# Performance work log

Hardware: AMD Instinct MI355X
Metric: run time of the kernel (lower is better)

## Reference

```python
import jax, jax.numpy as jnp
import numpy as np

N_NODES = 50000
N_EDGES = 800000
N_GRAPHS = 256
F_IN = 75  # num_features_xd


def _lin_params(key, fan_in, fan_out):
    kw, kb = jax.random.split(key)
    s = 1.0 / np.sqrt(fan_in)
    W = jax.random.uniform(kw, (fan_in, fan_out), jnp.float32, -s, s)
    b = jax.random.uniform(kb, (fan_out,), jnp.float32, -s, s)
    return W, b


def setup_inputs() -> dict:
    key = jax.random.key(0)
    ks = jax.random.split(key, 8)
    x = jax.random.normal(ks[0], (N_NODES, F_IN), jnp.float32)
    edge_index = jax.random.randint(ks[1], (2, N_EDGES), 0, N_NODES, jnp.int32)
    batch = jnp.sort(jax.random.randint(ks[2], (N_NODES,), 0, N_GRAPHS, jnp.int32))
    W1, b1 = _lin_params(ks[3], F_IN, F_IN)            # conv1: 75 -> 75
    W2, b2 = _lin_params(ks[4], F_IN, 2 * F_IN)        # conv2: 75 -> 150
    W3, b3 = _lin_params(ks[5], 2 * F_IN, 4 * F_IN)    # conv3: 150 -> 300
    Wg1, bg1 = _lin_params(ks[6], 4 * F_IN, 1024)      # fc_g1: 300 -> 1024
    Wg2, bg2 = _lin_params(ks[7], 1024, 128)           # fc_g2: 1024 -> 128
    return dict(x=x, edge_index=edge_index, batch=batch,
                W1=W1, b1=b1, W2=W2, b2=b2, W3=W3, b3=b3,
                Wg1=Wg1, bg1=bg1, Wg2=Wg2, bg2=bg2)


def gcn_conv(x, W, b, src, dst, n):
    """PyG GCNConv: out = D^{-1/2}(A+I)D^{-1/2} X W + b (symmetric norm, self loops)."""
    h = x @ W                                   # [n, out]
    loop = jnp.arange(n, dtype=src.dtype)
    s = jnp.concatenate([src, loop])            # [E+n]
    d = jnp.concatenate([dst, loop])
    deg = jax.ops.segment_sum(jnp.ones(s.shape[0], x.dtype), d, num_segments=n)
    dinv = jnp.where(deg > 0, jax.lax.rsqrt(jnp.maximum(deg, 1e-12)), 0.0)
    norm = dinv[s] * dinv[d]                    # [E+n]
    out = jax.ops.segment_sum(norm[:, None] * h[s], d, num_segments=n)
    return out + b


def reference(x, edge_index, batch, W1, b1, W2, b2, W3, b3, Wg1, bg1, Wg2, bg2):
    src, dst = edge_index[0], edge_index[1]
    n = x.shape[0]
    h = jax.nn.relu(gcn_conv(x, W1, b1, src, dst, n))
    h = jax.nn.relu(gcn_conv(h, W2, b2, src, dst, n))
    h = jax.nn.relu(gcn_conv(h, W3, b3, src, dst, n))
    g = jax.ops.segment_max(h, batch, num_segments=N_GRAPHS)  # global max pool
    g = jax.nn.relu(g @ Wg1 + bg1)
    # dropout is identity in eval mode
    return g @ Wg2 + bg2
```

## Files before the change

kernel.cpp:

```cpp
#include <hip/hip_runtime.h>
#include <math.h>

#define SCAN_B 1024
#define LDST 40

typedef __attribute__((ext_vector_type(8))) short short8v;
typedef __attribute__((ext_vector_type(8))) unsigned short ushort8v;
typedef __attribute__((ext_vector_type(4))) float f32x4;

static inline int ceil_div_i(long long a, int b) { return (int)((a + b - 1) / b); }

__device__ __forceinline__ unsigned short f2bf(float x) {
    unsigned int u = __float_as_uint(x);
    u += 0x7fffu + ((u >> 16) & 1u);
    return (unsigned short)(u >> 16);
}
__device__ __forceinline__ float bf2f(unsigned short h) {
    return __uint_as_float(((unsigned int)h) << 16);
}


__global__ __launch_bounds__(256) void k_count(const int* __restrict__ dst, int E,
                                               int* __restrict__ cnt) {
    int i = blockIdx.x * blockDim.x + threadIdx.x;
    if (i < E) atomicAdd(&cnt[dst[i]], 1);
}

__global__ __launch_bounds__(256) void k_dinv(const int* __restrict__ cnt,
                                              float* __restrict__ dinv, int N) {
    int i = blockIdx.x * blockDim.x + threadIdx.x;
    if (i < N) dinv[i] = (float)(1.0 / sqrt((double)(cnt[i] + 1)));
}

__global__ __launch_bounds__(256) void k_scan1(const int* __restrict__ cnt,
                                               int* __restrict__ rowptr,
                                               int* __restrict__ bsum, int N) {
    __shared__ int s[256];
    int tid = threadIdx.x;
    int base = blockIdx.x * SCAN_B + tid * 4;
    int a0 = (base + 0 < N) ? cnt[base + 0] : 0;
    int a1 = (base + 1 < N) ? cnt[base + 1] : 0;
    int a2 = (base + 2 < N) ? cnt[base + 2] : 0;
    int a3 = (base + 3 < N) ? cnt[base + 3] : 0;
    int tsum = a0 + a1 + a2 + a3;
    s[tid] = tsum;
    __syncthreads();
    for (int off = 1; off < 256; off <<= 1) {
        int val = 0;
        if (tid >= off) val = s[tid - off];
        __syncthreads();
        if (tid >= off) s[tid] += val;
        __syncthreads();
    }
    int texcl = s[tid] - tsum;
    if (tid == 255) bsum[blockIdx.x] = s[255];
    if (base + 0 < N) rowptr[base + 0] = texcl;
    if (base + 1 < N) rowptr[base + 1] = texcl + a0;
    if (base + 2 < N) rowptr[base + 2] = texcl + a0 + a1;
    if (base + 3 < N) rowptr[base + 3] = texcl + a0 + a1 + a2;
}

__global__ __launch_bounds__(256) void k_scan2(int* __restrict__ bsum, int NB) {
    __shared__ int s[256];
    int tid = threadIdx.x;
    int v = (tid < NB) ? bsum[tid] : 0;
    s[tid] = v;
    __syncthreads();
    for (int off = 1; off < 256; off <<= 1) {
        int val = 0;
        if (tid >= off) val = s[tid - off];
        __syncthreads();
        if (tid >= off) s[tid] += val;
        __syncthreads();
    }
    if (tid < NB) bsum[tid] = s[tid] - v;
}

__global__ __launch_bounds__(256) void k_scan3(int* __restrict__ rowptr,
                                               const int* __restrict__ bsum, int N, int E) {
    int i = blockIdx.x * blockDim.x + threadIdx.x;
    if (i < N) rowptr[i] += bsum[i >> 10];
    if (i == 0) rowptr[N] = E;
}

__global__ __launch_bounds__(256) void k_fill(const int* __restrict__ src,
                                              const int* __restrict__ dst, int E,
                                              const int* __restrict__ rowptr,
                                              int* __restrict__ fill,
                                              int* __restrict__ col) {
    int e = blockIdx.x * blockDim.x + threadIdx.x;
    if (e >= E) return;
    int s = src[e], d = dst[e];
    int pos = atomicAdd(&fill[d], 1);
    col[rowptr[d] + pos] = s;
}


__global__ __launch_bounds__(256) void k_xscale(const float* __restrict__ x,
                                                const float* __restrict__ dinv,
                                                unsigned short* __restrict__ xb,
                                                int N, int F, int XS) {
    int i = blockIdx.x * blockDim.x + threadIdx.x;
    int v = i / XS, c = i - v * XS;
    if (v >= N) return;
    float val = (c < F) ? dinv[v] * x[(size_t)v * F + c] : 0.f;
    xb[i] = f2bf(val);
}


template <int CHUNKS, int SLOTS, int UNR>
__global__ __launch_bounds__(256) void k_gather_s(const unsigned short* __restrict__ Xb,
                                                  const int* __restrict__ rowptr,
                                                  const int* __restrict__ col,
                                                  float* __restrict__ T, int N,
                                                  int XS, int KPf) {
    const int v = blockIdx.x * 4 + (threadIdx.x >> 6);
    const int lane = threadIdx.x & 63;
    if (v >= N) return;
    constexpr int VW = 8;
    const int slot = lane / CHUNKS;
    const int chunk = lane - slot * CHUNKS;
    const bool act = lane < CHUNKS * SLOTS;
    const int f0 = chunk * VW;

    float acc[VW];
#pragma unroll
    for (int u = 0; u < VW; u++) acc[u] = 0.f;
    if (slot == 0) {
        ushort8v h = *(const ushort8v*)(Xb + (size_t)v * XS + f0);
#pragma unroll
        for (int u = 0; u < VW; u++) acc[u] = bf2f(h[u]);
    }

    const int beg = rowptr[v], end = rowptr[v + 1];
    for (int jb = beg; jb < end; jb += 64) {
        const int nj = min(64, end - jb);
        int ec = 0;
        if (lane < nj) ec = col[jb + lane];
        for (int e = 0; e < nj; e += SLOTS * UNR) {
            int cs[UNR];
            bool vs[UNR];
#pragma unroll
            for (int u = 0; u < UNR; u++) {
                int srcl = e + u * SLOTS + slot;
                vs[u] = act && (srcl < nj);
                cs[u] = __shfl(ec, srcl & 63);
            }
            ushort8v xv[UNR];
#pragma unroll
            for (int u = 0; u < UNR; u++) {
#pragma unroll
                for (int k2 = 0; k2 < 8; k2++) xv[u][k2] = 0;
                if (vs[u]) xv[u] = *(const ushort8v*)(Xb + (size_t)cs[u] * XS + f0);
            }
#pragma unroll
            for (int u = 0; u < UNR; u++)
#pragma unroll
                for (int k2 = 0; k2 < VW; k2++)
                    acc[k2] += bf2f(xv[u][k2]);
        }
    }

#pragma unroll
    for (int k2 = 0; k2 < VW; k2++) {
        float t2 = acc[k2];
#pragma unroll
        for (int s2 = 1; s2 < SLOTS; s2++) t2 += __shfl(acc[k2], chunk + s2 * CHUNKS);
        acc[k2] = t2;
    }

    if (slot == 0 && f0 < KPf) {
        float* tv = T + (size_t)v * KPf + f0;
        f32x4 o0 = {acc[0], acc[1], acc[2], acc[3]};
        f32x4 o1 = {acc[4], acc[5], acc[6], acc[7]};
        *(f32x4*)tv = o0;
        *(f32x4*)(tv + 4) = o1;
    }
}


__global__ __launch_bounds__(256) void k_wsplit(const float* __restrict__ W,
                                                unsigned short* __restrict__ Wth,
                                                unsigned short* __restrict__ Wtl,
                                                int K, int Fout, int KP) {
    int i = blockIdx.x * blockDim.x + threadIdx.x;
    if (i >= Fout * KP) return;
    int c = i / KP, k = i - c * KP;
    float w = (k < K) ? W[(size_t)k * Fout + c] : 0.f;
    unsigned short h = f2bf(w);
    Wth[i] = h;
    Wtl[i] = f2bf(w - bf2f(h));
}


template <int MODE>
__global__ __launch_bounds__(256) void k_gemm_mfma(
    const float* __restrict__ A, int KPf,
    const unsigned short* __restrict__ Bth, const unsigned short* __restrict__ Btl,
    const float* __restrict__ bias, const float* __restrict__ dinvp,
    unsigned short* __restrict__ Cb, int CSbf,
    const int* __restrict__ batch, float* __restrict__ G,
    int N, int KP, int Fout) {
    __shared__ unsigned short sAh[128 * LDST];
    __shared__ unsigned short sAl[128 * LDST];
    __shared__ unsigned short sBh[128 * LDST];
    __shared__ unsigned short sBl[128 * LDST];
    __shared__ int sBatch[128];

    const int t = threadIdx.x;
    const int r0 = blockIdx.x * 128;
    const int c0 = blockIdx.y * 128;
    const int lane = t & 63;
    const int wv = t >> 6;
    const int wrow = (wv >> 1) * 64;
    const int wcol = (wv & 1) * 64;
    const int l15 = lane & 15;
    const int lk = (lane >> 4) * 8;
    const int nt = KP >> 5;

    const int srow = t >> 1;
    const int sseg = (t & 1) << 4;

    if (MODE == 1 && t < 128) sBatch[t] = (r0 + t < N) ? batch[r0 + t] : -1;

    const bool arow_ok = (r0 + srow) < N;
    const bool bcol_ok = (c0 + srow) < Fout;
    const float* aRow = A + (size_t)(r0 + srow) * KPf;
    const unsigned short* bhRow = Bth + (size_t)(c0 + srow) * KP;
    const unsigned short* blRow = Btl + (size_t)(c0 + srow) * KP;

    float av[16];
    ushort8v rbh0, rbh1, rbl0, rbl1;

    auto gload = [&](int kk) {
#pragma unroll
        for (int u = 0; u < 4; u++) {
            int gk = kk + sseg + u * 4;
            f32x4 f = {0.f, 0.f, 0.f, 0.f};
            if (arow_ok && gk < KPf) f = *(const f32x4*)&aRow[gk];
#pragma unroll
            for (int e = 0; e < 4; e++) av[u * 4 + e] = f[e];
        }
        if (bcol_ok) {
            const ushort8v* p = (const ushort8v*)&bhRow[kk + sseg];
            rbh0 = p[0];
            rbh1 = p[1];
            p = (const ushort8v*)&blRow[kk + sseg];
            rbl0 = p[0];
            rbl1 = p[1];
        } else {
#pragma unroll
            for (int e = 0; e < 8; e++) { rbh0[e] = 0; rbh1[e] = 0; rbl0[e] = 0; rbl1[e] = 0; }
        }
    };

    auto wlds = [&]() {
        int off = srow * LDST + sseg;
        ushort8v h0, h1, l0, l1;
#pragma unroll
        for (int e = 0; e < 8; e++) {
            unsigned short hh = f2bf(av[e]);
            h0[e] = hh;
            l0[e] = f2bf(av[e] - bf2f(hh));
        }
#pragma unroll
        for (int e = 0; e < 8; e++) {
            unsigned short hh = f2bf(av[8 + e]);
            h1[e] = hh;
            l1[e] = f2bf(av[8 + e] - bf2f(hh));
        }
        *(ushort8v*)&sAh[off] = h0;
        *(ushort8v*)&sAh[off + 8] = h1;
        *(ushort8v*)&sAl[off] = l0;
        *(ushort8v*)&sAl[off + 8] = l1;
        *(ushort8v*)&sBh[off] = rbh0;
        *(ushort8v*)&sBh[off + 8] = rbh1;
        *(ushort8v*)&sBl[off] = rbl0;
        *(ushort8v*)&sBl[off + 8] = rbl1;
    };

    f32x4 acc[4][4];
#pragma unroll
    for (int i = 0; i < 4; i++)
#pragma unroll
        for (int j = 0; j < 4; j++) acc[i][j] = (f32x4){0.f, 0.f, 0.f, 0.f};

    gload(0);
    for (int tc = 0; tc < nt; ++tc) {
        wlds();
        __syncthreads();
        if (tc + 1 < nt) gload((tc + 1) * 32);
        short8v ah[4], al[4];
#pragma unroll
        for (int i = 0; i < 4; i++) {
            int ro = (wrow + i * 16 + l15) * LDST + lk;
            ah[i] = *(const short8v*)&sAh[ro];
            al[i] = *(const short8v*)&sAl[ro];
        }
#pragma unroll
        for (int j = 0; j < 4; j++) {
            int co = (wcol + j * 16 + l15) * LDST + lk;
            short8v bh = *(const short8v*)&sBh[co];
            short8v bl = *(const short8v*)&sBl[co];
#pragma unroll
            for (int i = 0; i < 4; i++) {
                acc[i][j] = __builtin_amdgcn_mfma_f32_16x16x32_bf16(al[i], bh, acc[i][j], 0, 0, 0);
                acc[i][j] = __builtin_amdgcn_mfma_f32_16x16x32_bf16(ah[i], bl, acc[i][j], 0, 0, 0);
                acc[i][j] = __builtin_amdgcn_mfma_f32_16x16x32_bf16(ah[i], bh, acc[i][j], 0, 0, 0);
            }
        }
        __syncthreads();
    }

    float drw[16];
#pragma unroll
    for (int i = 0; i < 4; i++)
#pragma unroll
        for (int q = 0; q < 4; q++) {
            int gr = r0 + wrow + i * 16 + (lane >> 4) * 4 + q;
            drw[i * 4 + q] = (gr < N) ? dinvp[gr] : 0.f;
        }

    if (MODE == 0) {
#pragma unroll
        for (int j = 0; j < 4; j++) {
            int gc = c0 + wcol + j * 16 + l15;
            if (gc >= CSbf) continue;
            float bv = (gc < Fout) ? bias[gc] : 0.f;
#pragma unroll
            for (int i = 0; i < 4; i++) {
                int rb = r0 + wrow + i * 16 + (lane >> 4) * 4;
#pragma unroll
                for (int q = 0; q < 4; q++) {
                    int gr = rb + q;
                    if (gr >= N) continue;
                    float dr = drw[i * 4 + q];
                    float vv = (gc < Fout) ? fmaxf(fmaf(acc[i][j][q], dr, bv), 0.f) * dr : 0.f;
                    Cb[(size_t)gr * CSbf + gc] = f2bf(vv);
                }
            }
        }
    } else {
#pragma unroll
        for (int j = 0; j < 4; j++) {
            int gc = c0 + wcol + j * 16 + l15;
            if (gc >= Fout) continue;
            float bv = bias[gc];
            int gcur = -1;
            float vmax = 0.f;
#pragma unroll
            for (int i = 0; i < 4; i++) {
                int lr = wrow + i * 16 + (lane >> 4) * 4;
#pragma unroll
                for (int q = 0; q < 4; q++) {
                    int g = sBatch[lr + q];
                    float vv = fmaxf(fmaf(acc[i][j][q], drw[i * 4 + q], bv), 0.f);
                    if (g < 0) continue;
                    if (g != gcur) {
                        if (gcur >= 0)
                            atomicMax((int*)&G[(size_t)gcur * Fout + gc], __float_as_int(vmax));
                        gcur = g;
                        vmax = vv;
                    } else {
                        vmax = fmaxf(vmax, vv);
                    }
                }
            }
            if (gcur >= 0) atomicMax((int*)&G[(size_t)gcur * Fout + gc], __float_as_int(vmax));
        }
    }
}


__global__ __launch_bounds__(256) void k_fc1(const float* __restrict__ A,
                                             const float* __restrict__ W,
                                             const float* __restrict__ bias,
                                             float* __restrict__ C,
                                             int M, int K, int Nout) {
    __shared__ float sA[2 * 304];
    const int t = threadIdx.x;
    const int m0 = blockIdx.x * 2;
    const int oc = blockIdx.y * 256 + t;

    for (int i = t; i < 2 * K; i += 256) {
        int r = i / K, k = i - r * K;
        sA[r * 304 + k] = (m0 + r < M) ? A[(size_t)(m0 + r) * K + k] : 0.f;
    }
    __syncthreads();

    float acc0 = 0.f, acc1 = 0.f;
    int k = 0;
    for (; k + 8 <= K; k += 8) {
        float w[8];
#pragma unroll
        for (int u = 0; u < 8; u++) w[u] = W[(size_t)(k + u) * Nout + oc];
#pragma unroll
        for (int u = 0; u < 8; u++) {
            acc0 = fmaf(sA[k + u], w[u], acc0);
            acc1 = fmaf(sA[304 + k + u], w[u], acc1);
        }
    }
    for (; k < K; k++) {
        float w = W[(size_t)k * Nout + oc];
        acc0 = fmaf(sA[k], w, acc0);
        acc1 = fmaf(sA[304 + k], w, acc1);
    }
    float bv = bias[oc];
    if (m0 < M) C[(size_t)m0 * Nout + oc] = fmaxf(acc0 + bv, 0.f);
    if (m0 + 1 < M) C[(size_t)(m0 + 1) * Nout + oc] = fmaxf(acc1 + bv, 0.f);
}


__global__ __launch_bounds__(256) void k_fc2p(const float* __restrict__ A,
                                              const float* __restrict__ W,
                                              float* __restrict__ P,
                                              int M, int K, int Nout) {
    __shared__ float sA[2 * 256];
    const int t = threadIdx.x;
    const int m0 = blockIdx.x * 2;
    const int sk = blockIdx.y;
    const int k0 = sk * 256;
    const int row = t >> 7;
    const int oc = t & 127;

    for (int i = t; i < 2 * 256; i += 256) {
        int r = i >> 8, k = i & 255;
        sA[i] = (m0 + r < M) ? A[(size_t)(m0 + r) * K + k0 + k] : 0.f;
    }
    __syncthreads();

    const float* a = sA + row * 256;
    float acc = 0.f;
    for (int k = 0; k < 256; k += 8) {
        float w[8];
#pragma unroll
        for (int u = 0; u < 8; u++) w[u] = W[(size_t)(k0 + k + u) * Nout + oc];
#pragma unroll
        for (int u = 0; u < 8; u++) acc = fmaf(a[k + u], w[u], acc);
    }
    int m = m0 + row;
    if (m < M) P[((size_t)sk * M + m) * Nout + oc] = acc;
}

__global__ __launch_bounds__(256) void k_fc2r(const float* __restrict__ P,
                                              const float* __restrict__ bias,
                                              float* __restrict__ C,
                                              int M, int Nout, int SK) {
    int i = blockIdx.x * blockDim.x + threadIdx.x;
    if (i >= M * Nout) return;
    int oc = i % Nout;
    float acc = bias[oc];
    for (int s2 = 0; s2 < SK; s2++) acc += P[(size_t)s2 * M * Nout + i];
    C[i] = acc;
}


extern "C" void kernel_launch(void* const* d_in, const int* in_sizes, int n_in,
                              void* d_out, int out_size, void* d_ws, size_t ws_size,
                              hipStream_t stream) {
    const float* x     = (const float*)d_in[0];
    const int*   ei    = (const int*)d_in[1];
    const int*   batch = (const int*)d_in[2];
    const float* W1 = (const float*)d_in[3];
    const float* b1 = (const float*)d_in[4];
    const float* W2 = (const float*)d_in[5];
    const float* b2 = (const float*)d_in[6];
    const float* W3 = (const float*)d_in[7];
    const float* b3 = (const float*)d_in[8];
    const float* Wg1 = (const float*)d_in[9];
    const float* bg1 = (const float*)d_in[10];
    const float* Wg2 = (const float*)d_in[11];
    const float* bg2 = (const float*)d_in[12];

    const int N  = in_sizes[2];
    const int E  = in_sizes[1] / 2;
    const int F1 = in_sizes[4];
    const int F2 = in_sizes[6];
    const int F3 = in_sizes[8];
    const int H1 = in_sizes[10];
    const int OC = in_sizes[12];
    const int NG = out_size / OC;
    const int FIN = in_sizes[3] / F1;

    const int KP1 = 96,  KPf1 = 80;
    const int KP3 = 160, KPf3 = 152;
    const int XS0 = 80;
    const int HS1 = 80;
    const int HS2 = 152;

    const int* src = ei;
    const int* dst = ei + E;

    char* base = (char*)d_ws;
    size_t off = 0;
    auto alloc = [&](size_t bytes) -> void* {
        void* p = base + off;
        off = (off + bytes + 255) & ~(size_t)255;
        return p;
    };
    int*   cnt    = (int*)alloc((size_t)N * 4);
    int*   fill   = (int*)alloc((size_t)N * 4);
    int*   rowptr = (int*)alloc((size_t)(N + 1) * 4);
    float* dinv   = (float*)alloc((size_t)N * 4);
    int*   bsum   = (int*)alloc(256 * 4);
    int*   col    = (int*)alloc((size_t)E * 4);
    unsigned short* W1th = (unsigned short*)alloc((size_t)F1 * KP1 * 2);
    unsigned short* W1tl = (unsigned short*)alloc((size_t)F1 * KP1 * 2);
    unsigned short* W2th = (unsigned short*)alloc((size_t)F2 * KP1 * 2);
    unsigned short* W2tl = (unsigned short*)alloc((size_t)F2 * KP1 * 2);
    unsigned short* W3th = (unsigned short*)alloc((size_t)F3 * KP3 * 2);
    unsigned short* W3tl = (unsigned short*)alloc((size_t)F3 * KP3 * 2);
    float* Gb  = (float*)alloc((size_t)NG * F3 * 4);
    float* g1  = (float*)alloc((size_t)NG * H1 * 4);
    float* P2  = (float*)alloc((size_t)4 * NG * OC * 4);
    float* Tg  = (float*)alloc((size_t)N * KPf3 * 4);
    unsigned short* Xb  = (unsigned short*)alloc((size_t)N * XS0 * 2);
    unsigned short* H1b = (unsigned short*)alloc((size_t)N * HS1 * 2);
    unsigned short* H2b = (unsigned short*)alloc((size_t)N * HS2 * 2);

    hipMemsetAsync(cnt, 0, (size_t)N * 4, stream);
    hipMemsetAsync(fill, 0, (size_t)N * 4, stream);
    hipMemsetAsync(Gb, 0, (size_t)NG * F3 * 4, stream);

    k_count<<<ceil_div_i(E, 256), 256, 0, stream>>>(dst, E, cnt);
    k_dinv<<<ceil_div_i(N, 256), 256, 0, stream>>>(cnt, dinv, N);
    int NB = ceil_div_i(N, SCAN_B);
    k_scan1<<<NB, 256, 0, stream>>>(cnt, rowptr, bsum, N);
    k_scan2<<<1, 256, 0, stream>>>(bsum, NB);
    k_scan3<<<ceil_div_i(N, 256), 256, 0, stream>>>(rowptr, bsum, N, E);
    k_fill<<<ceil_div_i(E, 256), 256, 0, stream>>>(src, dst, E, rowptr, fill, col);

    k_wsplit<<<ceil_div_i((long long)F1 * KP1, 256), 256, 0, stream>>>(W1, W1th, W1tl, FIN, F1, KP1);
    k_wsplit<<<ceil_div_i((long long)F2 * KP1, 256), 256, 0, stream>>>(W2, W2th, W2tl, F1, F2, KP1);
    k_wsplit<<<ceil_div_i((long long)F3 * KP3, 256), 256, 0, stream>>>(W3, W3th, W3tl, F2, F3, KP3);
    k_xscale<<<ceil_div_i((long long)N * XS0, 256), 256, 0, stream>>>(x, dinv, Xb, N, FIN, XS0);

    dim3 blk(256);
    int gw = ceil_div_i(N, 4);
    int gx = ceil_div_i(N, 128);

    k_gather_s<10, 6, 2><<<gw, blk, 0, stream>>>(Xb, rowptr, col, Tg, N, XS0, KPf1);
    {
        dim3 g(gx, ceil_div_i(F1, 128));
        k_gemm_mfma<0><<<g, blk, 0, stream>>>(Tg, KPf1, W1th, W1tl, b1, dinv, H1b, HS1,
                                              nullptr, nullptr, N, KP1, F1);
    }
    k_gather_s<10, 6, 2><<<gw, blk, 0, stream>>>(H1b, rowptr, col, Tg, N, HS1, KPf1);
    {
        dim3 g(gx, ceil_div_i(F2, 128));
        k_gemm_mfma<0><<<g, blk, 0, stream>>>(Tg, KPf1, W2th, W2tl, b2, dinv, H2b, HS2,
                                              nullptr, nullptr, N, KP1, F2);
    }
    k_gather_s<19, 3, 4><<<gw, blk, 0, stream>>>(H2b, rowptr, col, Tg, N, HS2, KPf3);
    {
        dim3 g(gx, ceil_div_i(F3, 128));
        k_gemm_mfma<1><<<g, blk, 0, stream>>>(Tg, KPf3, W3th, W3tl, b3, dinv, nullptr, 0,
                                              batch, Gb, N, KP3, F3);
    }

    {
        dim3 g(ceil_div_i(NG, 2), H1 / 256);
        k_fc1<<<g, 256, 0, stream>>>(Gb, Wg1, bg1, g1, NG, F3, H1);
    }
    {
        dim3 g(ceil_div_i(NG, 2), 4);
        k_fc2p<<<g, 256, 0, stream>>>(g1, Wg2, P2, NG, H1, OC);
        k_fc2r<<<ceil_div_i((long long)NG * OC, 256), 256, 0, stream>>>(
            P2, bg2, (float*)d_out, NG, OC, 4);
    }
}
```

Baseline: 336.3 us.

## Emit bf16 hi/lo split from gather and use MFMA-fragment LDS layout in GEMM

```diff
diff --git a/kernel.cpp b/kernel.cpp
--- a/kernel.cpp
+++ b/kernel.cpp
@@ -2,7 +2,6 @@
 #include <math.h>
 
 #define SCAN_B 1024
-#define LDST 40
 
 typedef __attribute__((ext_vector_type(8))) short short8v;
 typedef __attribute__((ext_vector_type(8))) unsigned short ushort8v;
@@ -17,6 +16,12 @@
 }
 __device__ __forceinline__ float bf2f(unsigned short h) {
     return __uint_as_float(((unsigned int)h) << 16);
+}
+__device__ __forceinline__ ushort8v zero8() {
+    ushort8v z;
+#pragma unroll
+    for (int e = 0; e < 8; e++) z[e] = 0;
+    return z;
 }
 
 
@@ -112,8 +117,9 @@
 __global__ __launch_bounds__(256) void k_gather_s(const unsigned short* __restrict__ Xb,
                                                   const int* __restrict__ rowptr,
                                                   const int* __restrict__ col,
-                                                  float* __restrict__ T, int N,
-                                                  int XS, int KPf) {
+                                                  unsigned short* __restrict__ Th,
+                                                  unsigned short* __restrict__ Tl,
+                                                  int N, int XS, int KPf) {
     const int v = blockIdx.x * 4 + (threadIdx.x >> 6);
     const int lane = threadIdx.x & 63;
     if (v >= N) return;
@@ -149,8 +155,7 @@
             ushort8v xv[UNR];
 #pragma unroll
             for (int u = 0; u < UNR; u++) {
-#pragma unroll
-                for (int k2 = 0; k2 < 8; k2++) xv[u][k2] = 0;
+                xv[u] = zero8();
                 if (vs[u]) xv[u] = *(const ushort8v*)(Xb + (size_t)cs[u] * XS + f0);
             }
 #pragma unroll
@@ -170,11 +175,15 @@
     }
 
     if (slot == 0 && f0 < KPf) {
-        float* tv = T + (size_t)v * KPf + f0;
-        f32x4 o0 = {acc[0], acc[1], acc[2], acc[3]};
-        f32x4 o1 = {acc[4], acc[5], acc[6], acc[7]};
-        *(f32x4*)tv = o0;
-        *(f32x4*)(tv + 4) = o1;
+        ushort8v h8, l8;
+#pragma unroll
+        for (int u = 0; u < VW; u++) {
+            unsigned short hh = f2bf(acc[u]);
+            h8[u] = hh;
+            l8[u] = f2bf(acc[u] - bf2f(hh));
+        }
+        *(ushort8v*)(Th + (size_t)v * KPf + f0) = h8;
+        *(ushort8v*)(Tl + (size_t)v * KPf + f0) = l8;
     }
 }
 
@@ -195,16 +204,16 @@
 
 template <int MODE>
 __global__ __launch_bounds__(256) void k_gemm_mfma(
-    const float* __restrict__ A, int KPf,
+    const unsigned short* __restrict__ Ah, const unsigned short* __restrict__ Al, int KPf,
     const unsigned short* __restrict__ Bth, const unsigned short* __restrict__ Btl,
     const float* __restrict__ bias, const float* __restrict__ dinvp,
     unsigned short* __restrict__ Cb, int CSbf,
     const int* __restrict__ batch, float* __restrict__ G,
     int N, int KP, int Fout) {
-    __shared__ unsigned short sAh[128 * LDST];
-    __shared__ unsigned short sAl[128 * LDST];
-    __shared__ unsigned short sBh[128 * LDST];
-    __shared__ unsigned short sBl[128 * LDST];
+    __shared__ unsigned short sAh[128 * 32];
+    __shared__ unsigned short sAl[128 * 32];
+    __shared__ unsigned short sBh[128 * 32];
+    __shared__ unsigned short sBl[128 * 32];
     __shared__ int sBatch[128];
 
     const int t = threadIdx.x;
@@ -215,68 +224,53 @@
     const int wrow = (wv >> 1) * 64;
     const int wcol = (wv & 1) * 64;
     const int l15 = lane & 15;
-    const int lk = (lane >> 4) * 8;
     const int nt = KP >> 5;
 
     const int srow = t >> 1;
     const int sseg = (t & 1) << 4;
+    const int ltile = srow >> 4;
+    const int g0 = sseg >> 3;
+    const int wo0 = ltile * 512 + ((srow & 15) + 16 * g0) * 8;
+    const int wo1 = ltile * 512 + ((srow & 15) + 16 * (g0 + 1)) * 8;
 
     if (MODE == 1 && t < 128) sBatch[t] = (r0 + t < N) ? batch[r0 + t] : -1;
 
     const bool arow_ok = (r0 + srow) < N;
     const bool bcol_ok = (c0 + srow) < Fout;
-    const float* aRow = A + (size_t)(r0 + srow) * KPf;
+    const unsigned short* ahRow = Ah + (size_t)(r0 + srow) * KPf;
+    const unsigned short* alRow = Al + (size_t)(r0 + srow) * KPf;
     const unsigned short* bhRow = Bth + (size_t)(c0 + srow) * KP;
     const unsigned short* blRow = Btl + (size_t)(c0 + srow) * KP;
 
-    float av[16];
-    ushort8v rbh0, rbh1, rbl0, rbl1;
+    ushort8v rah0, rah1, ral0, ral1, rbh0, rbh1, rbl0, rbl1;
 
     auto gload = [&](int kk) {
-#pragma unroll
-        for (int u = 0; u < 4; u++) {
-            int gk = kk + sseg + u * 4;
-            f32x4 f = {0.f, 0.f, 0.f, 0.f};
-            if (arow_ok && gk < KPf) f = *(const f32x4*)&aRow[gk];
-#pragma unroll
-            for (int e = 0; e < 4; e++) av[u * 4 + e] = f[e];
-        }
+        int gk = kk + sseg;
+        bool ok0 = arow_ok && (gk < KPf);
+        bool ok1 = arow_ok && (gk + 8 < KPf);
+        rah0 = ok0 ? *(const ushort8v*)(ahRow + gk) : zero8();
+        rah1 = ok1 ? *(const ushort8v*)(ahRow + gk + 8) : zero8();
+        ral0 = ok0 ? *(const ushort8v*)(alRow + gk) : zero8();
+        ral1 = ok1 ? *(const ushort8v*)(alRow + gk + 8) : zero8();
         if (bcol_ok) {
-            const ushort8v* p = (const ushort8v*)&bhRow[kk + sseg];
-            rbh0 = p[0];
-            rbh1 = p[1];
-            p = (const ushort8v*)&blRow[kk + sseg];
-            rbl0 = p[0];
-            rbl1 = p[1];
+            rbh0 = *(const ushort8v*)(bhRow + gk);
+            rbh1 = *(const ushort8v*)(bhRow + gk + 8);
+            rbl0 = *(const ushort8v*)(blRow + gk);
+            rbl1 = *(const ushort8v*)(blRow + gk + 8);
         } else {
-#pragma unroll
-            for (int e = 0; e < 8; e++) { rbh0[e] = 0; rbh1[e] = 0; rbl0[e] = 0; rbl1[e] = 0; }
+            rbh0 = zero8(); rbh1 = zero8(); rbl0 = zero8(); rbl1 = zero8();
         }
     };
 
     auto wlds = [&]() {
-        int off = srow * LDST + sseg;
-        ushort8v h0, h1, l0, l1;
-#pragma unroll
-        for (int e = 0; e < 8; e++) {
-            unsigned short hh = f2bf(av[e]);
-            h0[e] = hh;
-            l0[e] = f2bf(av[e] - bf2f(hh));
-        }
-#pragma unroll
-        for (int e = 0; e < 8; e++) {
-            unsigned short hh = f2bf(av[8 + e]);
-            h1[e] = hh;
-            l1[e] = f2bf(av[8 + e] - bf2f(hh));
-        }
-        *(ushort8v*)&sAh[off] = h0;
-        *(ushort8v*)&sAh[off + 8] = h1;
-        *(ushort8v*)&sAl[off] = l0;
-        *(ushort8v*)&sAl[off + 8] = l1;
-        *(ushort8v*)&sBh[off] = rbh0;
-        *(ushort8v*)&sBh[off + 8] = rbh1;
-        *(ushort8v*)&sBl[off] = rbl0;
-        *(ushort8v*)&sBl[off + 8] = rbl1;
+        *(ushort8v*)&sAh[wo0] = rah0;
+        *(ushort8v*)&sAh[wo1] = rah1;
+        *(ushort8v*)&sAl[wo0] = ral0;
+        *(ushort8v*)&sAl[wo1] = ral1;
+        *(ushort8v*)&sBh[wo0] = rbh0;
+        *(ushort8v*)&sBh[wo1] = rbh1;
+        *(ushort8v*)&sBl[wo0] = rbl0;
+        *(ushort8v*)&sBl[wo1] = rbl1;
     };
 
     f32x4 acc[4][4];
@@ -284,6 +278,10 @@
     for (int i = 0; i < 4; i++)
 #pragma unroll
         for (int j = 0; j < 4; j++) acc[i][j] = (f32x4){0.f, 0.f, 0.f, 0.f};
+
+    const int atile = wrow >> 4;
+    const int btile = wcol >> 4;
+    const int lo = lane * 8;
 
     gload(0);
     for (int tc = 0; tc < nt; ++tc) {
@@ -293,15 +291,13 @@
         short8v ah[4], al[4];
 #pragma unroll
         for (int i = 0; i < 4; i++) {
-            int ro = (wrow + i * 16 + l15) * LDST + lk;
-            ah[i] = *(const short8v*)&sAh[ro];
-            al[i] = *(const short8v*)&sAl[ro];
+            ah[i] = *(const short8v*)&sAh[(atile + i) * 512 + lo];
+            al[i] = *(const short8v*)&sAl[(atile + i) * 512 + lo];
         }
 #pragma unroll
         for (int j = 0; j < 4; j++) {
-            int co = (wcol + j * 16 + l15) * LDST + lk;
-            short8v bh = *(const short8v*)&sBh[co];
-            short8v bl = *(const short8v*)&sBl[co];
+            short8v bh = *(const short8v*)&sBh[(btile + j) * 512 + lo];
+            short8v bl = *(const short8v*)&sBl[(btile + j) * 512 + lo];
 #pragma unroll
             for (int i = 0; i < 4; i++) {
                 acc[i][j] = __builtin_amdgcn_mfma_f32_16x16x32_bf16(al[i], bh, acc[i][j], 0, 0, 0);
@@ -513,7 +509,8 @@
     float* Gb  = (float*)alloc((size_t)NG * F3 * 4);
     float* g1  = (float*)alloc((size_t)NG * H1 * 4);
     float* P2  = (float*)alloc((size_t)4 * NG * OC * 4);
-    float* Tg  = (float*)alloc((size_t)N * KPf3 * 4);
+    unsigned short* TgH = (unsigned short*)alloc((size_t)N * KPf3 * 2);
+    unsigned short* TgL = (unsigned short*)alloc((size_t)N * KPf3 * 2);
     unsigned short* Xb  = (unsigned short*)alloc((size_t)N * XS0 * 2);
     unsigned short* H1b = (unsigned short*)alloc((size_t)N * HS1 * 2);
     unsigned short* H2b = (unsigned short*)alloc((size_t)N * HS2 * 2);
@@ -539,22 +536,22 @@
     int gw = ceil_div_i(N, 4);
     int gx = ceil_div_i(N, 128);
 
-    k_gather_s<10, 6, 2><<<gw, blk, 0, stream>>>(Xb, rowptr, col, Tg, N, XS0, KPf1);
+    k_gather_s<10, 6, 2><<<gw, blk, 0, stream>>>(Xb, rowptr, col, TgH, TgL, N, XS0, KPf1);
     {
         dim3 g(gx, ceil_div_i(F1, 128));
-        k_gemm_mfma<0><<<g, blk, 0, stream>>>(Tg, KPf1, W1th, W1tl, b1, dinv, H1b, HS1,
+        k_gemm_mfma<0><<<g, blk, 0, stream>>>(TgH, TgL, KPf1, W1th, W1tl, b1, dinv, H1b, HS1,
                                               nullptr, nullptr, N, KP1, F1);
     }
-    k_gather_s<10, 6, 2><<<gw, blk, 0, stream>>>(H1b, rowptr, col, Tg, N, HS1, KPf1);
+    k_gather_s<10, 6, 2><<<gw, blk, 0, stream>>>(H1b, rowptr, col, TgH, TgL, N, HS1, KPf1);
     {
         dim3 g(gx, ceil_div_i(F2, 128));
-        k_gemm_mfma<0><<<g, blk, 0, stream>>>(Tg, KPf1, W2th, W2tl, b2, dinv, H2b, HS2,
+        k_gemm_mfma<0><<<g, blk, 0, stream>>>(TgH, TgL, KPf1, W2th, W2tl, b2, dinv, H2b, HS2,
                                               nullptr, nullptr, N, KP1, F2);
     }
-    k_gather_s<19, 3, 4><<<gw, blk, 0, stream>>>(H2b, rowptr, col, Tg, N, HS2, KPf3);
+    k_gather_s<19, 3, 4><<<gw, blk, 0, stream>>>(H2b, rowptr, col, TgH, TgL, N, HS2, KPf3);
     {
         dim3 g(gx, ceil_div_i(F3, 128));
-        k_gemm_mfma<1><<<g, blk, 0, stream>>>(Tg, KPf3, W3th, W3tl, b3, dinv, nullptr, 0,
+        k_gemm_mfma<1><<<g, blk, 0, stream>>>(TgH, TgL, KPf3, W3th, W3tl, b3, dinv, nullptr, 0,
                                               batch, Gb, N, KP3, F3);
     }
 
```

New measurement: 350.3 us. 4.2% more time.
